# Kernel tuning notes

Measured on AMD Instinct MI355X. Metric: run time of the kernel, lower is better.

Reference implementation:

```python
import jax, jax.numpy as jnp
import numpy as np

L, B, S, D, H = 6, 2, 2048, 512, 8
DH = D // H
FF = 4 * D
EPS = 1e-5


def setup_inputs() -> dict:
    key = jax.random.key(0)
    ks = jax.random.split(key, 10)
    w = lambda k, shape: jax.random.normal(k, shape, jnp.float32) * 0.02
    return {
        "query": jax.random.normal(ks[0], (B, S, D), jnp.float32),
        "key": jax.random.normal(ks[1], (B, S, D), jnp.float32),
        "query_mask": jnp.ones((B, S), jnp.int32),
        "key_mask": jnp.ones((B, S), jnp.int32),
        # per-layer stacked params; conv1d(kernel=1) == linear with weight [out,in]
        "Wq": w(ks[2], (L, D, D)), "bq": jnp.zeros((L, D), jnp.float32),
        "Wk": w(ks[3], (L, D, D)), "bk": jnp.zeros((L, D), jnp.float32),
        "Wv": w(ks[4], (L, D, D)), "bv": jnp.zeros((L, D), jnp.float32),
        "Wo": w(ks[5], (L, D, D)), "bo": jnp.zeros((L, D), jnp.float32),
        "ln1_g": jnp.ones((L, D), jnp.float32), "ln1_b": jnp.zeros((L, D), jnp.float32),
        "ff_w1": w(ks[6], (L, FF, D)), "ff_b1": jnp.zeros((L, FF), jnp.float32),
        "ff_w2": w(ks[7], (L, D, FF)), "ff_b2": jnp.zeros((L, D), jnp.float32),
        "ln2_g": jnp.ones((L, D), jnp.float32), "ln2_b": jnp.zeros((L, D), jnp.float32),
    }


def _layer_norm(x, g, b):
    m = jnp.mean(x, axis=-1, keepdims=True)
    v = jnp.mean(jnp.square(x - m), axis=-1, keepdims=True)
    return (x - m) * jax.lax.rsqrt(v + EPS) * g + b


def reference(query, key, query_mask, key_mask,
              Wq, bq, Wk, bk, Wv, bv, Wo, bo,
              ln1_g, ln1_b, ff_w1, ff_b1, ff_w2, ff_b2, ln2_g, ln2_b):
    b_, s_, d_ = query.shape
    kpad = (key_mask == 0)[:, None, None, :]          # [B,1,1,K]
    qm = query_mask.astype(query.dtype)[:, :, None]    # [B,S,1]
    x = query
    for i in range(L):
        # QKV projections (conv1d kernel-size-1 == linear), split heads -> [B,H,S,DH]
        def split(t):
            return t.reshape(b_, s_, H, DH).transpose(0, 2, 1, 3)
        q = split(x @ Wq[i].T + bq[i]) * (float(DH) ** -0.5)
        k = split(key @ Wk[i].T + bk[i])
        v = split(key @ Wv[i].T + bv[i])
        attn = jnp.einsum('bhqd,bhkd->bhqk', q, k)
        attn = jnp.where(kpad, -jnp.inf, attn)
        attn = jax.nn.softmax(attn, axis=-1)
        o = jnp.einsum('bhqk,bhkd->bhqd', attn, v)
        o = o.transpose(0, 2, 1, 3).reshape(b_, s_, H * DH)
        o = (o @ Wo[i].T + bo[i]) * qm                 # output proj + query mask
        x = _layer_norm(o + x, ln1_g[i], ln1_b[i])
        h = jax.nn.leaky_relu(x @ ff_w1[i].T + ff_b1[i], 0.01)
        f = (h @ ff_w2[i].T + ff_b2[i]) * qm           # FFN mask on output
        x = _layer_norm(f + x, ln2_g[i], ln2_b[i])
    return x
```

## Files before the change

kernel.cpp:

```cpp
#include <hip/hip_runtime.h>
#include <stdint.h>

constexpr int LAYERS = 6;
constexpr int Bc = 2, Sc = 2048, Dc = 512, Hc = 8, DHc = 64, FFc = 2048;
constexpr int Mc = Bc * Sc;
constexpr int NS = 2;
constexpr int KCHUNK = Sc / NS;

typedef __attribute__((ext_vector_type(8))) __bf16 bf16x8;
typedef __attribute__((ext_vector_type(4))) __bf16 bf16x4;
typedef __attribute__((ext_vector_type(4))) float f32x4;

__device__ __forceinline__ void async_ld16(const void* g, void* lds) {
  __builtin_amdgcn_global_load_lds(
      (const __attribute__((address_space(1))) uint32_t*)g,
      (__attribute__((address_space(3))) uint32_t*)lds, 16, 0, 0);
}

__global__ __launch_bounds__(256) void cvt_all(
    const float* __restrict__ Wq, const float* __restrict__ Wo,
    const float* __restrict__ fw1, const float* __restrict__ fw2,
    const float* __restrict__ query, const float* __restrict__ key,
    __bf16* __restrict__ wq_b, __bf16* __restrict__ wo_b,
    __bf16* __restrict__ w1_b, __bf16* __restrict__ w2_b,
    __bf16* __restrict__ x_b, __bf16* __restrict__ key_b,
    float* __restrict__ x_f) {
  size_t i = ((size_t)blockIdx.x * 256 + threadIdx.x) * 4;
  constexpr size_t nW = (size_t)LAYERS * Dc * Dc;
  constexpr size_t nF = (size_t)LAYERS * FFc * Dc;
  constexpr size_t nX = (size_t)Mc * Dc;
  const float* src;
  __bf16* dst;
  float* fdst = nullptr;
  if (i < nW) { src = Wq + i; dst = wq_b + i; }
  else if (i < 2 * nW) { size_t j = i - nW; src = Wo + j; dst = wo_b + j; }
  else if (i < 2 * nW + nF) { size_t j = i - 2 * nW; src = fw1 + j; dst = w1_b + j; }
  else if (i < 2 * nW + 2 * nF) { size_t j = i - 2 * nW - nF; src = fw2 + j; dst = w2_b + j; }
  else if (i < 2 * nW + 2 * nF + nX) {
    size_t j = i - 2 * nW - 2 * nF;
    src = query + j; dst = x_b + j; fdst = x_f + j;
  } else {
    size_t j = i - 2 * nW - 2 * nF - nX;
    src = key + j; dst = key_b + j;
  }
  const float4 v = *(const float4*)src;
  bf16x4 o;
  o[0] = (__bf16)v.x; o[1] = (__bf16)v.y; o[2] = (__bf16)v.z; o[3] = (__bf16)v.w;
  *(bf16x4*)dst = o;
  if (fdst) *(float4*)fdst = v;
}

__global__ __launch_bounds__(256) void cvt_kv_kernel(const float* __restrict__ Wk,
                                                     const float* __restrict__ Wv,
                                                     __bf16* __restrict__ out) {
  size_t i = ((size_t)blockIdx.x * 256 + threadIdx.x) * 4;
  int n = (int)(i / ((size_t)Dc * Dc));
  int lyr = n >> 1, p = n & 1;
  size_t idx = i - (size_t)n * Dc * Dc;
  const float* src = (p ? Wv : Wk) + (size_t)lyr * Dc * Dc + idx;
  const float4 v = *(const float4*)src;
  bf16x4 o;
  o[0] = (__bf16)v.x; o[1] = (__bf16)v.y; o[2] = (__bf16)v.z; o[3] = (__bf16)v.w;
  *(bf16x4*)(out + i) = o;
}

__global__ __launch_bounds__(256) void kbias_kernel(const int* __restrict__ km,
                                                    float* __restrict__ kb, int n) {
  int i = blockIdx.x * 256 + threadIdx.x;
  if (i < n) kb[i] = km[i] ? 0.f : -1e30f;
}

template <int BM, int BN, int WM, int WN, int EPI>
__global__ __launch_bounds__(256) void gemm_bt(
    const __bf16* __restrict__ A, const __bf16* __restrict__ W,
    const float* __restrict__ bias, const float* __restrict__ bias2,
    float* __restrict__ outf, __bf16* __restrict__ outb,
    __bf16* __restrict__ outb2, float scale,
    int M, int N, int K, int Kstride) {
  constexpr int BK = 64;
  __shared__ __bf16 As[2][BM * BK];
  __shared__ __bf16 Bs[2][BN * BK];
  const int tid = threadIdx.x;
  const int l15 = tid & 15;
  const int lg = (tid & 63) >> 4;
  const int w = tid >> 6;
  const int wm = w >> 1, wn = w & 1;
  const int tm = blockIdx.y * BM;
  const int tn = blockIdx.x * BN;
  const int z = blockIdx.z;
  const __bf16* Ap = A + (size_t)tm * Kstride + (size_t)z * K;
  const __bf16* Wp = W + (size_t)tn * Kstride + (size_t)z * K;
  f32x4 acc[WM][WN] = {};

  auto stage = [&](int k0, int bf) {
#pragma unroll
    for (int c = 0; c < BM * 8 / 256; ++c) {
      int cc = c * 256 + tid;
      int r = cc >> 3, s = cc & 7;
      int ss = s ^ (r & 7);
      async_ld16(Ap + (size_t)r * Kstride + k0 + ss * 8, &As[bf][cc * 8]);
    }
#pragma unroll
    for (int c = 0; c < BN * 8 / 256; ++c) {
      int cc = c * 256 + tid;
      int r = cc >> 3, s = cc & 7;
      int ss = s ^ (r & 7);
      async_ld16(Wp + (size_t)r * Kstride + k0 + ss * 8, &Bs[bf][cc * 8]);
    }
  };

  const int nk = K / BK;
  stage(0, 0);
  __syncthreads();
  int buf = 0;
  for (int t = 0; t < nk; ++t) {
    if (t + 1 < nk) stage((t + 1) * BK, buf ^ 1);
    bf16x8 af[WM][2], bfr[WN][2];
#pragma unroll
    for (int i = 0; i < WM; ++i) {
      int row = wm * WM * 16 + i * 16 + l15;
#pragma unroll
      for (int kf = 0; kf < 2; ++kf)
        af[i][kf] = *(const bf16x8*)&As[buf][row * 64 + (((kf * 4 + lg) ^ (row & 7)) * 8)];
    }
#pragma unroll
    for (int j = 0; j < WN; ++j) {
      int row = wn * WN * 16 + j * 16 + l15;
#pragma unroll
      for (int kf = 0; kf < 2; ++kf)
        bfr[j][kf] = *(const bf16x8*)&Bs[buf][row * 64 + (((kf * 4 + lg) ^ (row & 7)) * 8)];
    }
#pragma unroll
    for (int kf = 0; kf < 2; ++kf)
#pragma unroll
      for (int i = 0; i < WM; ++i)
#pragma unroll
        for (int j = 0; j < WN; ++j)
          acc[i][j] = __builtin_amdgcn_mfma_f32_16x16x32_bf16(af[i][kf], bfr[j][kf], acc[i][j], 0, 0, 0);
    __syncthreads();
    buf ^= 1;
  }

  if constexpr (EPI == 6) {
    const bool isV = ((tn & 1023) >= 512);
    const int lyr = tn >> 10;
    const int b = tm >> 11;
    const int sbase = tm & (Sc - 1);
    if (isV) {
      __bf16* T = (__bf16*)&As[0][0];
#pragma unroll
      for (int i = 0; i < WM; ++i) {
#pragma unroll
        for (int j = 0; j < WN; ++j) {
          const int d = wn * WN * 16 + j * 16 + l15;
          const int dg = (tn & 511) + d;
          const float bv = bias2[lyr * 512 + dg];
          const int s0 = wm * WM * 16 + i * 16 + lg * 4;
          bf16x4 pk;
#pragma unroll
          for (int r = 0; r < 4; ++r) pk[r] = (__bf16)(acc[i][j][r] + bv);
          const int slot = (s0 >> 3) ^ (d & 7);
          *(bf16x4*)&T[d * 64 + slot * 8 + (s0 & 7)] = pk;
        }
      }
      __syncthreads();
      const int rr = tid >> 3;
      const int c8 = tid & 7;
#pragma unroll
      for (int pass = 0; pass < 4; ++pass) {
        const int d = pass * 32 + rr;
        const int slot = c8 ^ (d & 7);
        bf16x8 v8 = *(const bf16x8*)&T[d * 64 + slot * 8];
        const int dg = (tn & 511) + d;
        const int h = dg >> 6, dh = dg & 63;
        *(bf16x8*)&outb2[((((size_t)(lyr * Bc + b) * Hc + h)) * DHc + dh) * Sc +
                         sbase + c8 * 8] = v8;
      }
    } else {
#pragma unroll
      for (int i = 0; i < WM; ++i) {
#pragma unroll
        for (int j = 0; j < WN; ++j) {
          const int d = wn * WN * 16 + j * 16 + l15;
          const int dg = (tn & 511) + d;
          const float bv = bias[lyr * 512 + dg];
          const int h = dg >> 6, dh = dg & 63;
#pragma unroll
          for (int r = 0; r < 4; ++r) {
            const int s = sbase + wm * WM * 16 + i * 16 + lg * 4 + r;
            outb[((((size_t)(lyr * Bc + b) * Hc + h)) * Sc + s) * DHc + dh] =
                (__bf16)(acc[i][j][r] + bv);
          }
        }
      }
    }
    return;
  }

#pragma unroll
  for (int i = 0; i < WM; ++i) {
#pragma unroll
    for (int j = 0; j < WN; ++j) {
      const int n = tn + wn * WN * 16 + j * 16 + l15;
      float bv;
      if constexpr (EPI == 0) {
        bv = (z == 0) ? bias[n] : 0.f;
      } else {
        bv = bias[n];
      }
#pragma unroll
      for (int r = 0; r < 4; ++r) {
        const int m = tm + wm * WM * 16 + i * 16 + lg * 4 + r;
        float v = acc[i][j][r] + bv;
        if constexpr (EPI == 0) {
          outf[(size_t)z * M * N + (size_t)m * N + n] = v;
        } else if constexpr (EPI == 1) {
          int b = m >> 11, s = m & (Sc - 1);
          int h = n >> 6, dh = n & 63;
          outb[(((size_t)(b * Hc + h)) * Sc + s) * DHc + dh] = (__bf16)(v * scale);
        } else if constexpr (EPI == 4) {
          float lv = v > 0.f ? v : 0.01f * v;
          outb[(size_t)m * N + n] = (__bf16)lv;
        }
      }
    }
  }
}

__global__ __launch_bounds__(512, 2) void attn_kernel(
    const __bf16* __restrict__ q, const __bf16* __restrict__ k,
    const __bf16* __restrict__ vt, const float* __restrict__ kb,
    __bf16* __restrict__ Opart, float* __restrict__ mpart,
    float* __restrict__ lpart) {
  const int bid = blockIdx.x;
  const int o = (bid & 7) * 64 + (bid >> 3);
  const int qb = o & 15;
  const int p = o >> 4;
  const int bh = p >> 1;
  const int z = p & 1;
  const int b = bh >> 3;
  const int w = threadIdx.x >> 6;
  const int l = threadIdx.x & 63;
  const int l15 = l & 15;
  const int lg = l >> 4;
  const int tid = threadIdx.x;
  const int qbase = qb * 128 + w * 16;
  const int k0 = z * KCHUNK;

  const __bf16* qp = q + ((size_t)bh * Sc + qbase) * DHc;
  const __bf16* kp = k + (size_t)bh * Sc * DHc;
  const __bf16* vp = vt + (size_t)bh * DHc * Sc;
  const float* kbp = kb + (size_t)b * Sc;

  bf16x8 qf[2];
  qf[0] = *(const bf16x8*)(qp + l15 * DHc + lg * 8);
  qf[1] = *(const bf16x8*)(qp + l15 * DHc + 32 + lg * 8);

  bf16x8 onesf;
#pragma unroll
  for (int i = 0; i < 8; ++i) onesf[i] = (__bf16)1.0f;

  f32x4 oacc[4] = {};
  f32x4 lacc = {};
  float mr = -1e30f;

  __shared__ __bf16 Ks[2][4096];
  __shared__ __bf16 Vs[2][4096];

  auto stage = [&](int t, int bf) {
    const int kt = k0 + t * 64;
    int i = tid;
    int r = i >> 3;
    int bsrc = (i & 7) ^ (r & 7);
    async_ld16(kp + (size_t)(kt + r) * DHc + bsrc * 8, &Ks[bf][i * 8]);
    async_ld16(vp + (size_t)r * Sc + kt + bsrc * 8, &Vs[bf][i * 8]);
  };

  stage(0, 0);
  __syncthreads();

  constexpr int NT = KCHUNK / 64;
  int buf = 0;
  for (int t = 0; t < NT; ++t) {
    const int kt = k0 + t * 64;
    if (t + 1 < NT) stage(t + 1, buf ^ 1);

    float4 mb4[4];
#pragma unroll
    for (int cb = 0; cb < 4; ++cb)
      mb4[cb] = *(const float4*)&kbp[kt + cb * 16 + lg * 4];

    f32x4 sacc[4] = {};
    __builtin_amdgcn_s_setprio(1);
#pragma unroll
    for (int kf = 0; kf < 2; ++kf) {
#pragma unroll
      for (int cb = 0; cb < 4; ++cb) {
        int row = cb * 16 + l15;
        bf16x8 kfr = *(const bf16x8*)&Ks[buf][row * 64 + (((kf * 4 + lg) ^ (row & 7)) * 8)];
        sacc[cb] = __builtin_amdgcn_mfma_f32_16x16x32_bf16(kfr, qf[kf], sacc[cb], 0, 0, 0);
      }
    }
    __builtin_amdgcn_s_setprio(0);
    sacc[0][0] += mb4[0].x; sacc[0][1] += mb4[0].y; sacc[0][2] += mb4[0].z; sacc[0][3] += mb4[0].w;
    sacc[1][0] += mb4[1].x; sacc[1][1] += mb4[1].y; sacc[1][2] += mb4[1].z; sacc[1][3] += mb4[1].w;
    sacc[2][0] += mb4[2].x; sacc[2][1] += mb4[2].y; sacc[2][2] += mb4[2].z; sacc[2][3] += mb4[2].w;
    sacc[3][0] += mb4[3].x; sacc[3][1] += mb4[3].y; sacc[3][2] += mb4[3].z; sacc[3][3] += mb4[3].w;

    float mx = sacc[0][0];
#pragma unroll
    for (int cb = 0; cb < 4; ++cb)
#pragma unroll
      for (int r = 0; r < 4; ++r) mx = fmaxf(mx, sacc[cb][r]);
    mx = fmaxf(mx, __shfl_xor(mx, 16, 64));
    mx = fmaxf(mx, __shfl_xor(mx, 32, 64));

    if (__any(mx > mr + 8.f)) {
      float mn = fmaxf(mr, mx);
      float f = __expf(mr - mn);
      mr = mn;
      float fj[4];
#pragma unroll
      for (int j = 0; j < 4; ++j) fj[j] = __shfl(f, lg * 4 + j, 64);
#pragma unroll
      for (int j = 0; j < 4; ++j) lacc[j] *= fj[j];
#pragma unroll
      for (int db = 0; db < 4; ++db)
#pragma unroll
        for (int j = 0; j < 4; ++j) oacc[db][j] *= fj[j];
    }

    unsigned pw[4][2];
#pragma unroll
    for (int cb = 0; cb < 4; ++cb) {
#pragma unroll
      for (int w2 = 0; w2 < 2; ++w2) {
        union { __bf16 h[2]; unsigned u; } cu;
        cu.h[0] = (__bf16)__expf(sacc[cb][2 * w2] - mr);
        cu.h[1] = (__bf16)__expf(sacc[cb][2 * w2 + 1] - mr);
        pw[cb][w2] = cu.u;
      }
    }

    const int srcA = ((lg & 1) * 2) * 16 + l15;
    const int srcB = srcA + 16;
    const bool hi = (lg >> 1) & 1;
#pragma unroll
    for (int kf = 0; kf < 2; ++kf) {
      unsigned t0a = __shfl((int)pw[kf * 2][0], srcA, 64);
      unsigned t0b = __shfl((int)pw[kf * 2 + 1][0], srcA, 64);
      unsigned t1a = __shfl((int)pw[kf * 2][1], srcA, 64);
      unsigned t1b = __shfl((int)pw[kf * 2 + 1][1], srcA, 64);
      unsigned t2a = __shfl((int)pw[kf * 2][0], srcB, 64);
      unsigned t2b = __shfl((int)pw[kf * 2 + 1][0], srcB, 64);
      unsigned t3a = __shfl((int)pw[kf * 2][1], srcB, 64);
      unsigned t3b = __shfl((int)pw[kf * 2 + 1][1], srcB, 64);
      union { unsigned u[4]; bf16x8 v; } pa;
      pa.u[0] = hi ? t0b : t0a;
      pa.u[1] = hi ? t1b : t1a;
      pa.u[2] = hi ? t2b : t2a;
      pa.u[3] = hi ? t3b : t3a;
      __builtin_amdgcn_s_setprio(1);
      lacc = __builtin_amdgcn_mfma_f32_16x16x32_bf16(pa.v, onesf, lacc, 0, 0, 0);
#pragma unroll
      for (int db = 0; db < 4; ++db) {
        int row = db * 16 + l15;
        bf16x8 vf = *(const bf16x8*)&Vs[buf][row * 64 + (((kf * 4 + lg) ^ (row & 7)) * 8)];
        oacc[db] = __builtin_amdgcn_mfma_f32_16x16x32_bf16(pa.v, vf, oacc[db], 0, 0, 0);
      }
      __builtin_amdgcn_s_setprio(0);
    }
    __syncthreads();
    buf ^= 1;
  }

  const size_t obase = (((size_t)(z * Bc * Hc + bh)) * Sc + qbase) * DHc;
#pragma unroll
  for (int db = 0; db < 4; ++db)
#pragma unroll
    for (int j = 0; j < 4; ++j)
      Opart[obase + (size_t)(lg * 4 + j) * DHc + db * 16 + l15] = (__bf16)oacc[db][j];
  const int row0 = (z * Bc * Hc + bh) * Sc + qbase;
  if (lg == 0) mpart[row0 + l15] = mr;
  if (l15 == 0) {
#pragma unroll
    for (int j = 0; j < 4; ++j) lpart[row0 + lg * 4 + j] = lacc[j];
  }
}

__global__ __launch_bounds__(256) void attn_combine(
    const __bf16* __restrict__ Opart, const float* __restrict__ mpart,
    const float* __restrict__ lpart, __bf16* __restrict__ out) {
  int t = blockIdx.x * 256 + threadIdx.x;
  int g = t & 7;
  int row = t >> 3;
  int bh = row >> 11, s = row & (Sc - 1);
  constexpr int RSTRIDE = Bc * Hc * Sc;
  float m0 = mpart[row], m1 = mpart[RSTRIDE + row];
  float l0 = lpart[row], l1 = lpart[RSTRIDE + row];
  float M = fmaxf(m0, m1);
  float e0 = __expf(m0 - M), e1 = __expf(m1 - M);
  float inv = 1.0f / (e0 * l0 + e1 * l1);
  bf16x8 o0 = *(const bf16x8*)&Opart[(size_t)row * DHc + g * 8];
  bf16x8 o1 = *(const bf16x8*)&Opart[((size_t)RSTRIDE + row) * DHc + g * 8];
  bf16x8 r;
#pragma unroll
  for (int e = 0; e < 8; ++e)
    r[e] = (__bf16)((e0 * (float)o0[e] + e1 * (float)o1[e]) * inv);
  int b = bh >> 3, h = bh & 7;
  *(bf16x8*)&out[(((size_t)b * Sc + s)) * Dc + h * DHc + g * 8] = r;
}

__global__ __launch_bounds__(256) void add_ln_kernel(
    const float* __restrict__ res, const float* __restrict__ res2,
    const int* __restrict__ rmask, const float* __restrict__ xin,
    const float* __restrict__ g, const float* __restrict__ bb,
    float* __restrict__ xo, __bf16* __restrict__ xbo) {
  const int tid = threadIdx.x;
  const int rl = tid >> 7;
  const int row = blockIdx.x * 2 + rl;
  const int ci = (tid & 127) * 4;
  const size_t base = (size_t)row * Dc + ci;
  const float4 a = *(const float4*)(res + base);
  const float4 a2 = *(const float4*)(res2 + base);
  const float4 xv = *(const float4*)(xin + base);
  const float mfac = (float)rmask[row];
  float4 v;
  v.x = (a.x + a2.x) * mfac + xv.x;
  v.y = (a.y + a2.y) * mfac + xv.y;
  v.z = (a.z + a2.z) * mfac + xv.z;
  v.w = (a.w + a2.w) * mfac + xv.w;
  float s = v.x + v.y + v.z + v.w;
#pragma unroll
  for (int d = 1; d < 64; d <<= 1) s += __shfl_xor(s, d, 64);
  __shared__ float red[4], red2[4];
  if ((tid & 63) == 0) red[tid >> 6] = s;
  __syncthreads();
  float mean = (red[rl * 2] + red[rl * 2 + 1]) * (1.0f / Dc);
  float4 dv;
  dv.x = v.x - mean; dv.y = v.y - mean; dv.z = v.z - mean; dv.w = v.w - mean;
  float qq = dv.x * dv.x + dv.y * dv.y + dv.z * dv.z + dv.w * dv.w;
#pragma unroll
  for (int d = 1; d < 64; d <<= 1) qq += __shfl_xor(qq, d, 64);
  if ((tid & 63) == 0) red2[tid >> 6] = qq;
  __syncthreads();
  float var = (red2[rl * 2] + red2[rl * 2 + 1]) * (1.0f / Dc);
  float rs = rsqrtf(var + 1e-5f);
  const float4 gv = *(const float4*)(g + ci);
  const float4 bv = *(const float4*)(bb + ci);
  float4 ov;
  ov.x = dv.x * rs * gv.x + bv.x;
  ov.y = dv.y * rs * gv.y + bv.y;
  ov.z = dv.z * rs * gv.z + bv.z;
  ov.w = dv.w * rs * gv.w + bv.w;
  *(float4*)(xo + base) = ov;
  bf16x4 ob;
  ob[0] = (__bf16)ov.x; ob[1] = (__bf16)ov.y; ob[2] = (__bf16)ov.z; ob[3] = (__bf16)ov.w;
  *(bf16x4*)(xbo + base) = ob;
}

extern "C" void kernel_launch(void* const* d_in, const int* in_sizes, int n_in,
                              void* d_out, int out_size, void* d_ws, size_t ws_size,
                              hipStream_t stream) {
  (void)in_sizes; (void)n_in; (void)out_size; (void)ws_size;
  const float* query = (const float*)d_in[0];
  const float* key   = (const float*)d_in[1];
  const int* qmask   = (const int*)d_in[2];
  const int* kmask   = (const int*)d_in[3];
  const float* Wq = (const float*)d_in[4];
  const float* bq = (const float*)d_in[5];
  const float* Wk = (const float*)d_in[6];
  const float* bk = (const float*)d_in[7];
  const float* Wv = (const float*)d_in[8];
  const float* bv = (const float*)d_in[9];
  const float* Wo = (const float*)d_in[10];
  const float* bo = (const float*)d_in[11];
  const float* ln1g = (const float*)d_in[12];
  const float* ln1b = (const float*)d_in[13];
  const float* fw1 = (const float*)d_in[14];
  const float* fb1 = (const float*)d_in[15];
  const float* fw2 = (const float*)d_in[16];
  const float* fb2 = (const float*)d_in[17];
  const float* ln2g = (const float*)d_in[18];
  const float* ln2b = (const float*)d_in[19];

  char* ws = (char*)d_ws;
  size_t off = 0;
  auto carve = [&](size_t bytes) -> void* {
    void* p = ws + off;
    off += (bytes + 255) & ~(size_t)255;
    return p;
  };
  float* x_f    = (float*)carve((size_t)Mc * Dc * 4);
  float* tmp_f  = (float*)carve((size_t)2 * Mc * Dc * 4);
  __bf16* x_b   = (__bf16*)carve((size_t)Mc * Dc * 2);
  __bf16* key_b = (__bf16*)carve((size_t)Mc * Dc * 2);
  __bf16* q_b   = (__bf16*)carve((size_t)Mc * Dc * 2);
  __bf16* at_b  = (__bf16*)carve((size_t)Mc * Dc * 2);
  __bf16* h_b   = (__bf16*)carve((size_t)Mc * FFc * 2);
  __bf16* k_all = (__bf16*)carve((size_t)LAYERS * Mc * Dc * 2);
  __bf16* vt_all= (__bf16*)carve((size_t)LAYERS * Mc * Dc * 2);
  __bf16* wq_b  = (__bf16*)carve((size_t)LAYERS * Dc * Dc * 2);
  __bf16* wkv_b = (__bf16*)carve((size_t)LAYERS * 2 * Dc * Dc * 2);
  __bf16* wo_b  = (__bf16*)carve((size_t)LAYERS * Dc * Dc * 2);
  __bf16* w1_b  = (__bf16*)carve((size_t)LAYERS * FFc * Dc * 2);
  __bf16* w2_b  = (__bf16*)carve((size_t)LAYERS * Dc * FFc * 2);
  float* ml_f   = (float*)carve((size_t)NS * Bc * Hc * Sc * 4 * 2);
  float* kb_f   = (float*)carve((size_t)Bc * Sc * 4);

  __bf16* opart_b = h_b;
  float* mpart_f = ml_f;
  float* lpart_f = ml_f + (size_t)NS * Bc * Hc * Sc;
  float* tmp2_f = tmp_f + (size_t)Mc * Dc;

  cvt_all<<<19456, 256, 0, stream>>>(Wq, Wo, fw1, fw2, query, key,
                                     wq_b, wo_b, w1_b, w2_b, x_b, key_b, x_f);
  cvt_kv_kernel<<<LAYERS * 2 * Dc * Dc / 1024, 256, 0, stream>>>(Wk, Wv, wkv_b);
  kbias_kernel<<<Bc * Sc / 256, 256, 0, stream>>>(kmask, kb_f, Bc * Sc);

  const dim3 blk(256);
  const dim3 blkA(512);
  const dim3 gP64(Dc / 64, Mc / 64);
  const dim3 gOP(Dc / 64, Mc / 64, 2);
  const dim3 gFF2(Dc / 64, Mc / 64, 2);
  const dim3 gKV(LAYERS * 2 * Dc / 128, Mc / 64);
  const dim3 gFF1(FFc / 128, Mc / 64);
  const dim3 gAttn(Sc / 128 * Bc * Hc * NS);
  const dim3 gComb(Bc * Hc * Sc * 8 / 256);
  const dim3 gLN(Mc / 2);

  gemm_bt<64, 128, 2, 4, 6><<<gKV, blk, 0, stream>>>(
      key_b, wkv_b, bk, bv, nullptr, k_all, vt_all, 1.0f,
      Mc, LAYERS * 2 * Dc, Dc, Dc);

  for (int i = 0; i < LAYERS; ++i) {
    const __bf16* wq_i = wq_b + (size_t)i * Dc * Dc;
    const __bf16* wo_i = wo_b + (size_t)i * Dc * Dc;
    const __bf16* w1_i = w1_b + (size_t)i * FFc * Dc;
    const __bf16* w2_i = w2_b + (size_t)i * Dc * FFc;
    const __bf16* k_i  = k_all + (size_t)i * Mc * Dc;
    const __bf16* vt_i = vt_all + (size_t)i * Mc * Dc;

    gemm_bt<64, 64, 2, 2, 1><<<gP64, blk, 0, stream>>>(
        x_b, wq_i, bq + i * Dc, nullptr, nullptr, q_b, nullptr, 0.125f,
        Mc, Dc, Dc, Dc);
    attn_kernel<<<gAttn, blkA, 0, stream>>>(q_b, k_i, vt_i, kb_f,
                                            opart_b, mpart_f, lpart_f);
    attn_combine<<<gComb, blk, 0, stream>>>(opart_b, mpart_f, lpart_f, at_b);
    gemm_bt<64, 64, 2, 2, 0><<<gOP, blk, 0, stream>>>(
        at_b, wo_i, bo + i * Dc, nullptr, tmp_f, nullptr, nullptr, 1.0f,
        Mc, Dc, Dc / 2, Dc);
    add_ln_kernel<<<gLN, blk, 0, stream>>>(tmp_f, tmp2_f, qmask, x_f,
                                           ln1g + i * Dc, ln1b + i * Dc, x_f, x_b);
    gemm_bt<64, 128, 2, 4, 4><<<gFF1, blk, 0, stream>>>(
        x_b, w1_i, fb1 + i * FFc, nullptr, nullptr, h_b, nullptr, 1.0f,
        Mc, FFc, Dc, Dc);
    gemm_bt<64, 64, 2, 2, 0><<<gFF2, blk, 0, stream>>>(
        h_b, w2_i, fb2 + i * Dc, nullptr, tmp_f, nullptr, nullptr, 1.0f,
        Mc, Dc, FFc / 2, FFc);
    add_ln_kernel<<<gLN, blk, 0, stream>>>(tmp_f, tmp2_f, qmask, x_f,
                                           ln2g + i * Dc, ln2b + i * Dc, x_f, x_b);
  }
  hipMemcpyAsync(d_out, x_f, (size_t)Mc * Dc * 4, hipMemcpyDeviceToDevice, stream);
}
```

Before: 762.7 us.

## Stage 128-key tiles in attention and alternate FFN1 GEMM tile shapes across layers

The attention kernel now stages 128 keys per pipeline step instead of 64. It processes them as two 64-key halves, so barriers and stage calls happen half as often. The V tile uses a 128-wide row with a 16-slot XOR swizzle. Even layers now run the FFN1 GEMM with a 64x64 tile config and odd layers keep 64x128, which looks like an A/B experiment across layers. The larger shared-memory footprint (64KB per block) may reduce attention occupancy.

```diff
diff --git a/kernel.cpp b/kernel.cpp
--- a/kernel.cpp
+++ b/kernel.cpp
@@ -264,111 +264,120 @@
   f32x4 lacc = {};
   float mr = -1e30f;
 
-  __shared__ __bf16 Ks[2][4096];
-  __shared__ __bf16 Vs[2][4096];
+  __shared__ __bf16 Ks[2][8192];
+  __shared__ __bf16 Vs[2][8192];
 
   auto stage = [&](int t, int bf) {
-    const int kt = k0 + t * 64;
-    int i = tid;
-    int r = i >> 3;
-    int bsrc = (i & 7) ^ (r & 7);
-    async_ld16(kp + (size_t)(kt + r) * DHc + bsrc * 8, &Ks[bf][i * 8]);
-    async_ld16(vp + (size_t)r * Sc + kt + bsrc * 8, &Vs[bf][i * 8]);
+    const int kt = k0 + t * 128;
+#pragma unroll
+    for (int ii = 0; ii < 2; ++ii) {
+      int i = ii * 512 + tid;
+      int r = i >> 3;
+      int ss = (i & 7) ^ (r & 7);
+      async_ld16(kp + (size_t)(kt + r) * DHc + ss * 8, &Ks[bf][i * 8]);
+      int d = i >> 4;
+      int vs = (i & 15) ^ (d & 15);
+      async_ld16(vp + (size_t)d * Sc + kt + vs * 8, &Vs[bf][i * 8]);
+    }
   };
 
   stage(0, 0);
   __syncthreads();
 
-  constexpr int NT = KCHUNK / 64;
+  constexpr int NT = KCHUNK / 128;
   int buf = 0;
   for (int t = 0; t < NT; ++t) {
-    const int kt = k0 + t * 64;
     if (t + 1 < NT) stage(t + 1, buf ^ 1);
-
-    float4 mb4[4];
-#pragma unroll
-    for (int cb = 0; cb < 4; ++cb)
-      mb4[cb] = *(const float4*)&kbp[kt + cb * 16 + lg * 4];
-
-    f32x4 sacc[4] = {};
-    __builtin_amdgcn_s_setprio(1);
-#pragma unroll
-    for (int kf = 0; kf < 2; ++kf) {
+#pragma unroll
+    for (int h2 = 0; h2 < 2; ++h2) {
+      const int kt = k0 + t * 128 + h2 * 64;
+
+      float4 mb4[4];
+#pragma unroll
+      for (int cb = 0; cb < 4; ++cb)
+        mb4[cb] = *(const float4*)&kbp[kt + cb * 16 + lg * 4];
+
+      f32x4 sacc[4] = {};
+      __builtin_amdgcn_s_setprio(1);
+#pragma unroll
+      for (int kf = 0; kf < 2; ++kf) {
+#pragma unroll
+        for (int cb = 0; cb < 4; ++cb) {
+          int row = h2 * 64 + cb * 16 + l15;
+          bf16x8 kfr = *(const bf16x8*)&Ks[buf][row * 64 + (((kf * 4 + lg) ^ (row & 7)) * 8)];
+          sacc[cb] = __builtin_amdgcn_mfma_f32_16x16x32_bf16(kfr, qf[kf], sacc[cb], 0, 0, 0);
+        }
+      }
+      __builtin_amdgcn_s_setprio(0);
+      sacc[0][0] += mb4[0].x; sacc[0][1] += mb4[0].y; sacc[0][2] += mb4[0].z; sacc[0][3] += mb4[0].w;
+      sacc[1][0] += mb4[1].x; sacc[1][1] += mb4[1].y; sacc[1][2] += mb4[1].z; sacc[1][3] += mb4[1].w;
+      sacc[2][0] += mb4[2].x; sacc[2][1] += mb4[2].y; sacc[2][2] += mb4[2].z; sacc[2][3] += mb4[2].w;
+      sacc[3][0] += mb4[3].x; sacc[3][1] += mb4[3].y; sacc[3][2] += mb4[3].z; sacc[3][3] += mb4[3].w;
+
+      float mx = sacc[0][0];
+#pragma unroll
+      for (int cb = 0; cb < 4; ++cb)
+#pragma unroll
+        for (int r = 0; r < 4; ++r) mx = fmaxf(mx, sacc[cb][r]);
+      mx = fmaxf(mx, __shfl_xor(mx, 16, 64));
+      mx = fmaxf(mx, __shfl_xor(mx, 32, 64));
+
+      if (__any(mx > mr + 8.f)) {
+        float mn = fmaxf(mr, mx);
+        float f = __expf(mr - mn);
+        mr = mn;
+        float fj[4];
+#pragma unroll
+        for (int j = 0; j < 4; ++j) fj[j] = __shfl(f, lg * 4 + j, 64);
+#pragma unroll
+        for (int j = 0; j < 4; ++j) lacc[j] *= fj[j];
+#pragma unroll
+        for (int db = 0; db < 4; ++db)
+#pragma unroll
+          for (int j = 0; j < 4; ++j) oacc[db][j] *= fj[j];
+      }
+
+      unsigned pw[4][2];
 #pragma unroll
       for (int cb = 0; cb < 4; ++cb) {
-        int row = cb * 16 + l15;
-        bf16x8 kfr = *(const bf16x8*)&Ks[buf][row * 64 + (((kf * 4 + lg) ^ (row & 7)) * 8)];
-        sacc[cb] = __builtin_amdgcn_mfma_f32_16x16x32_bf16(kfr, qf[kf], sacc[cb], 0, 0, 0);
-      }
-    }
-    __builtin_amdgcn_s_setprio(0);
-    sacc[0][0] += mb4[0].x; sacc[0][1] += mb4[0].y; sacc[0][2] += mb4[0].z; sacc[0][3] += mb4[0].w;
-    sacc[1][0] += mb4[1].x; sacc[1][1] += mb4[1].y; sacc[1][2] += mb4[1].z; sacc[1][3] += mb4[1].w;
-    sacc[2][0] += mb4[2].x; sacc[2][1] += mb4[2].y; sacc[2][2] += mb4[2].z; sacc[2][3] += mb4[2].w;
-    sacc[3][0] += mb4[3].x; sacc[3][1] += mb4[3].y; sacc[3][2] += mb4[3].z; sacc[3][3] += mb4[3].w;
-
-    float mx = sacc[0][0];
-#pragma unroll
-    for (int cb = 0; cb < 4; ++cb)
-#pragma unroll
-      for (int r = 0; r < 4; ++r) mx = fmaxf(mx, sacc[cb][r]);
-    mx = fmaxf(mx, __shfl_xor(mx, 16, 64));
-    mx = fmaxf(mx, __shfl_xor(mx, 32, 64));
-
-    if (__any(mx > mr + 8.f)) {
-      float mn = fmaxf(mr, mx);
-      float f = __expf(mr - mn);
-      mr = mn;
-      float fj[4];
-#pragma unroll
-      for (int j = 0; j < 4; ++j) fj[j] = __shfl(f, lg * 4 + j, 64);
-#pragma unroll
-      for (int j = 0; j < 4; ++j) lacc[j] *= fj[j];
-#pragma unroll
-      for (int db = 0; db < 4; ++db)
-#pragma unroll
-        for (int j = 0; j < 4; ++j) oacc[db][j] *= fj[j];
-    }
-
-    unsigned pw[4][2];
-#pragma unroll
-    for (int cb = 0; cb < 4; ++cb) {
-#pragma unroll
-      for (int w2 = 0; w2 < 2; ++w2) {
-        union { __bf16 h[2]; unsigned u; } cu;
-        cu.h[0] = (__bf16)__expf(sacc[cb][2 * w2] - mr);
-        cu.h[1] = (__bf16)__expf(sacc[cb][2 * w2 + 1] - mr);
-        pw[cb][w2] = cu.u;
-      }
-    }
-
-    const int srcA = ((lg & 1) * 2) * 16 + l15;
-    const int srcB = srcA + 16;
-    const bool hi = (lg >> 1) & 1;
-#pragma unroll
-    for (int kf = 0; kf < 2; ++kf) {
-      unsigned t0a = __shfl((int)pw[kf * 2][0], srcA, 64);
-      unsigned t0b = __shfl((int)pw[kf * 2 + 1][0], srcA, 64);
-      unsigned t1a = __shfl((int)pw[kf * 2][1], srcA, 64);
-      unsigned t1b = __shfl((int)pw[kf * 2 + 1][1], srcA, 64);
-      unsigned t2a = __shfl((int)pw[kf * 2][0], srcB, 64);
-      unsigned t2b = __shfl((int)pw[kf * 2 + 1][0], srcB, 64);
-      unsigned t3a = __shfl((int)pw[kf * 2][1], srcB, 64);
-      unsigned t3b = __shfl((int)pw[kf * 2 + 1][1], srcB, 64);
-      union { unsigned u[4]; bf16x8 v; } pa;
-      pa.u[0] = hi ? t0b : t0a;
-      pa.u[1] = hi ? t1b : t1a;
-      pa.u[2] = hi ? t2b : t2a;
-      pa.u[3] = hi ? t3b : t3a;
-      __builtin_amdgcn_s_setprio(1);
-      lacc = __builtin_amdgcn_mfma_f32_16x16x32_bf16(pa.v, onesf, lacc, 0, 0, 0);
-#pragma unroll
-      for (int db = 0; db < 4; ++db) {
-        int row = db * 16 + l15;
-        bf16x8 vf = *(const bf16x8*)&Vs[buf][row * 64 + (((kf * 4 + lg) ^ (row & 7)) * 8)];
-        oacc[db] = __builtin_amdgcn_mfma_f32_16x16x32_bf16(pa.v, vf, oacc[db], 0, 0, 0);
-      }
-      __builtin_amdgcn_s_setprio(0);
+#pragma unroll
+        for (int w2 = 0; w2 < 2; ++w2) {
+          union { __bf16 h[2]; unsigned u; } cu;
+          cu.h[0] = (__bf16)__expf(sacc[cb][2 * w2] - mr);
+          cu.h[1] = (__bf16)__expf(sacc[cb][2 * w2 + 1] - mr);
+          pw[cb][w2] = cu.u;
+        }
+      }
+
+      const int srcA = ((lg & 1) * 2) * 16 + l15;
+      const int srcB = srcA + 16;
+      const bool hi = (lg >> 1) & 1;
+#pragma unroll
+      for (int kf = 0; kf < 2; ++kf) {
+        unsigned t0a = __shfl((int)pw[kf * 2][0], srcA, 64);
+        unsigned t0b = __shfl((int)pw[kf * 2 + 1][0], srcA, 64);
+        unsigned t1a = __shfl((int)pw[kf * 2][1], srcA, 64);
+        unsigned t1b = __shfl((int)pw[kf * 2 + 1][1], srcA, 64);
+        unsigned t2a = __shfl((int)pw[kf * 2][0], srcB, 64);
+        unsigned t2b = __shfl((int)pw[kf * 2 + 1][0], srcB, 64);
+        unsigned t3a = __shfl((int)pw[kf * 2][1], srcB, 64);
+        unsigned t3b = __shfl((int)pw[kf * 2 + 1][1], srcB, 64);
+        union { unsigned u[4]; bf16x8 v; } pa;
+        pa.u[0] = hi ? t0b : t0a;
+        pa.u[1] = hi ? t1b : t1a;
+        pa.u[2] = hi ? t2b : t2a;
+        pa.u[3] = hi ? t3b : t3a;
+        __builtin_amdgcn_s_setprio(1);
+        lacc = __builtin_amdgcn_mfma_f32_16x16x32_bf16(pa.v, onesf, lacc, 0, 0, 0);
+#pragma unroll
+        for (int db = 0; db < 4; ++db) {
+          int d = db * 16 + l15;
+          int slot = (h2 * 8 + kf * 4 + lg) ^ (d & 15);
+          bf16x8 vf = *(const bf16x8*)&Vs[buf][d * 128 + slot * 8];
+          oacc[db] = __builtin_amdgcn_mfma_f32_16x16x32_bf16(pa.v, vf, oacc[db], 0, 0, 0);
+        }
+        __builtin_amdgcn_s_setprio(0);
+      }
     }
     __syncthreads();
     buf ^= 1;
@@ -524,7 +533,8 @@
   const dim3 gOP(Dc / 64, Mc / 64, 2);
   const dim3 gFF2(Dc / 64, Mc / 64, 2);
   const dim3 gKV(LAYERS * 2 * Dc / 128, Mc / 64);
-  const dim3 gFF1(FFc / 128, Mc / 64);
+  const dim3 gFF1a(FFc / 64, Mc / 64);
+  const dim3 gFF1b(FFc / 128, Mc / 64);
   const dim3 gAttn(Sc / 128 * Bc * Hc * NS);
   const dim3 gComb(Bc * Hc * Sc * 8 / 256);
   const dim3 gLN(Mc / 2);
@@ -552,9 +562,14 @@
         Mc, Dc, Dc / 2, Dc);
     add_ln_kernel<<<gLN, blk, 0, stream>>>(tmp_f, tmp2_f, qmask, x_f,
                                            ln1g + i * Dc, ln1b + i * Dc, x_f, x_b);
-    gemm_bt<64, 128, 2, 4, 4><<<gFF1, blk, 0, stream>>>(
-        x_b, w1_i, fb1 + i * FFc, nullptr, nullptr, h_b, nullptr, 1.0f,
-        Mc, FFc, Dc, Dc);
+    if (i & 1)
+      gemm_bt<64, 128, 2, 4, 4><<<gFF1b, blk, 0, stream>>>(
+          x_b, w1_i, fb1 + i * FFc, nullptr, nullptr, h_b, nullptr, 1.0f,
+          Mc, FFc, Dc, Dc);
+    else
+      gemm_bt<64, 64, 2, 2, 4><<<gFF1a, blk, 0, stream>>>(
+          x_b, w1_i, fb1 + i * FFc, nullptr, nullptr, h_b, nullptr, 1.0f,
+          Mc, FFc, Dc, Dc);
     gemm_bt<64, 64, 2, 2, 0><<<gFF2, blk, 0, stream>>>(
         h_b, w2_i, fb2 + i * Dc, nullptr, tmp_f, nullptr, nullptr, 1.0f,
         Mc, Dc, FFc / 2, FFc);
```

New measurement: 751.0 us. No clear change (-1.5%).
